# Kernel optimization log

Hardware: AMD Instinct MI355X
Metric: run time of the kernel (lower is better)

Reference implementation:

```python
import jax, jax.numpy as jnp
import numpy as np

K = 16  # kNN size (self included)
R = 4   # upsampling ratio


def _knn(pts, k):
    # pts: (B,N,3) -> idx (B,N,k); smallest distance first, so idx[:,:,0] is self
    sq = jnp.sum(pts * pts, axis=-1)
    d = sq[:, :, None] - 2.0 * jnp.einsum('bnd,bmd->bnm', pts, pts) + sq[:, None, :]
    _, idx = jax.lax.top_k(-d, k)
    return idx


def _gather(feats, idx):
    # feats (B,N,C), idx (B,N,k) -> (B,N,k,C)
    return jax.vmap(lambda f, i: f[i])(feats, idx)


def _conv1d(x, w, b):  # pointwise Conv1d: x (B,C,N)
    return jnp.einsum('oc,bcn->bon', w, x) + b[None, :, None]


def _conv2d(x, w, b):  # pointwise Conv2d: x (B,C,N,K)
    return jnp.einsum('oc,bcnk->bonk', w, x) + b[None, :, None, None]


def setup_inputs() -> dict:
    key = jax.random.key(0)
    ks = jax.random.split(key, 16)
    B, N = 2, 8192
    w = lambda k, s: jax.random.normal(k, s, jnp.float32) * 0.1
    return {
        'x': jax.random.normal(ks[0], (B, 3, N), jnp.float32),
        'mlp1_w1': w(ks[1], (32, 3)), 'mlp1_b1': jnp.zeros((32,), jnp.float32),
        'mlp1_w2': w(ks[2], (64, 32)), 'mlp1_b2': jnp.zeros((64,), jnp.float32),
        'mlp2_w1': w(ks[3], (32, 9)), 'mlp2_b1': jnp.zeros((32,), jnp.float32),
        'mlp3_w1': w(ks[4], (128, 96)), 'mlp3_b1': jnp.zeros((128,), jnp.float32),
        'mlp3_w2': w(ks[5], (12, 128)), 'mlp3_b2': jnp.zeros((12,), jnp.float32),
        'att_w1': w(ks[6], (128, 64)), 'att_b1': jnp.zeros((128,), jnp.float32),
        'att_w2': w(ks[7], (64, 128)), 'att_b2': jnp.zeros((64,), jnp.float32),
    }


def reference(x, mlp1_w1, mlp1_b1, mlp1_w2, mlp1_b2, mlp2_w1, mlp2_b1,
              mlp3_w1, mlp3_b1, mlp3_w2, mlp3_b2,
              att_w1, att_b1, att_w2, att_b2):
    B, C, N = x.shape
    pts = jnp.transpose(x, (0, 2, 1))                     # (B,N,3)
    idx = _knn(jax.lax.stop_gradient(pts), K)             # (B,N,K)

    # local 3x3 covariance features -> (B,9,N)
    nb = _gather(pts, idx)                                # (B,N,K,3)
    c = nb - jnp.mean(nb, axis=2, keepdims=True)
    cov = jnp.einsum('bnki,bnkj->bnij', c, c) / K         # (B,N,3,3)
    cov_feat = jnp.transpose(cov.reshape(B, N, 9), (0, 2, 1))

    # mlp1: 3 -> 32 -> 64, relu on both (last_act=True)
    f1 = jax.nn.relu(_conv1d(jax.nn.relu(_conv1d(x, mlp1_w1, mlp1_b1)), mlp1_w2, mlp1_b2))

    # gather neighbor features (exclude self) and form relative features
    fk = _gather(jnp.transpose(f1, (0, 2, 1)), idx[:, :, 1:])   # (B,N,K-1,64)
    f_knn = jnp.transpose(fk, (0, 3, 1, 2)) - f1[:, :, :, None]  # (B,64,N,K-1)

    # attention MLP (2D): 64 -> 128 -> 64, softmax over neighbor axis
    h = jax.nn.relu(_conv2d(f_knn, att_w1, att_b1))
    w = jax.nn.softmax(_conv2d(h, att_w2, att_b2), axis=-1)
    f_agg = jnp.sum(w * f_knn, axis=-1)                   # (B,64,N)

    # mlp2: 9 -> 32 with relu
    f_cov = jax.nn.relu(_conv1d(cov_feat, mlp2_w1, mlp2_b1))     # (B,32,N)

    f = jnp.concatenate([f_agg, f_cov], axis=1)           # (B,96,N)
    g = _conv1d(jax.nn.relu(_conv1d(f, mlp3_w1, mlp3_b1)), mlp3_w2, mlp3_b2)  # (B,3R,N)

    return jnp.tile(x, (1, 1, R)) + 0.15 * g.reshape(B, -1, R * N)
```

## Files before the change

### kernel.cpp

```cpp
#include <hip/hip_runtime.h>

#define BB 2
#define NN 8192
#define KK 16
#define QPB 64
#define PRE 256
#define CAP 10
typedef unsigned long long ull;
typedef unsigned short ushort;
#define KINF 0xFFFFFFFFFFFFFFFFULL

typedef __attribute__((ext_vector_type(8))) short short8;
typedef __attribute__((ext_vector_type(4))) float f32x4;

static __device__ __forceinline__ ushort f2bf(float f) {
    unsigned u = __float_as_uint(f);
    unsigned r = (u + 0x7FFFu + ((u >> 16) & 1u)) >> 16;
    return (ushort)r;
}
static __device__ __forceinline__ float bf2f(ushort s) {
    return __uint_as_float(((unsigned)s) << 16);
}

static __device__ __forceinline__ float distq(const float4& qp, const float4& cn) {
    return fmaf(qp.x, cn.x, fmaf(qp.y, cn.y, fmaf(qp.z, cn.z, __fadd_rn(qp.w, cn.w))));
}

__global__ __launch_bounds__(256) void prep_f1_kernel(
    const float* __restrict__ x, float4* __restrict__ pts4, float4* __restrict__ pts4n,
    const float* __restrict__ w1, const float* __restrict__ b1,
    const float* __restrict__ w2, const float* __restrict__ b2,
    ushort* __restrict__ f1)
{
    if (blockIdx.x < 64) {
        int t = blockIdx.x * 256 + threadIdx.x;
        int b = t >> 13, n = t & (NN - 1);
        float x0 = x[(b * 3 + 0) * NN + n];
        float x1 = x[(b * 3 + 1) * NN + n];
        float x2 = x[(b * 3 + 2) * NN + n];
        float sq = fmaf(x2, x2, fmaf(x1, x1, __fmul_rn(x0, x0)));
        pts4[t]  = make_float4(x0, x1, x2, sq);
        pts4n[t] = make_float4(-2.f * x0, -2.f * x1, -2.f * x2, sq);
    } else {
        int P = (blockIdx.x - 64) * 256 + threadIdx.x;
        int b = P >> 13, n = P & (NN - 1);
        float x0 = x[(b * 3 + 0) * NN + n];
        float x1 = x[(b * 3 + 1) * NN + n];
        float x2 = x[(b * 3 + 2) * NN + n];
        float h[32];
#pragma unroll
        for (int o = 0; o < 32; ++o) {
            float v = fmaf(w1[o * 3 + 2], x2, fmaf(w1[o * 3 + 1], x1, fmaf(w1[o * 3 + 0], x0, b1[o])));
            h[o] = fmaxf(v, 0.f);
        }
#pragma unroll
        for (int o4 = 0; o4 < 16; ++o4) {
            float vv[4];
#pragma unroll
            for (int u = 0; u < 4; ++u) {
                int o = o4 * 4 + u;
                float v = b2[o];
#pragma unroll
                for (int k = 0; k < 32; ++k) v = fmaf(w2[o * 32 + k], h[k], v);
                vv[u] = fmaxf(v, 0.f);
            }
            ushort4 s = { f2bf(vv[0]), f2bf(vv[1]), f2bf(vv[2]), f2bf(vv[3]) };
            *(ushort4*)(f1 + (size_t)P * 64 + o4 * 4) = s;
        }
    }
}

__global__ __launch_bounds__(512) void knn_prefix_kernel(
    const float4* __restrict__ pts4, const float4* __restrict__ pts4n,
    float* __restrict__ thrb)
{
    __shared__ float smem[8 * 4 * 64];

    const int t    = threadIdx.x;
    const int wv   = t >> 6;
    const int lane = t & 63;
    const int b    = blockIdx.y;
    const int q    = blockIdx.x * QPB + lane;
    const int sl   = __builtin_amdgcn_readfirstlane(wv);

    const float4 qp = pts4[b * NN + q];
    const float4* __restrict__ cp = pts4n + (size_t)b * NN + (size_t)sl * 1024;

    float l0 = 3.0e38f, l1 = 3.0e38f, l2 = 3.0e38f, l3 = 3.0e38f;

    for (int i0 = 0; i0 < PRE; i0 += 8) {
#pragma unroll
        for (int u = 0; u < 8; ++u) {
            float d = distq(qp, cp[i0 + u]);
            if (d < l3) {
                bool b2 = d < l2, b1 = d < l1, b0 = d < l0;
                l3 = b2 ? l2 : d;
                l2 = b2 ? (b1 ? l1 : d) : l2;
                l1 = b1 ? (b0 ? l0 : d) : l1;
                l0 = b0 ? d : l0;
            }
        }
    }

    smem[(wv * 4 + 0) * 64 + lane] = l0;
    smem[(wv * 4 + 1) * 64 + lane] = l1;
    smem[(wv * 4 + 2) * 64 + lane] = l2;
    smem[(wv * 4 + 3) * 64 + lane] = l3;
    __syncthreads();

    if (t < QPB) {
        float h[8];
        int kc[8];
#pragma unroll
        for (int s = 0; s < 8; ++s) { h[s] = smem[(s * 4) * 64 + t]; kc[s] = 0; }
        float best = 3.0e38f;
        for (int o = 0; o < KK; ++o) {
            best = h[0]; int bs = 0;
#pragma unroll
            for (int s = 1; s < 8; ++s) { if (h[s] < best) { best = h[s]; bs = s; } }
#pragma unroll
            for (int s = 0; s < 8; ++s) {
                if (s == bs) {
                    kc[s]++;
                    h[s] = (kc[s] < 4) ? smem[(s * 4 + kc[s]) * 64 + t] : 3.0e38f;
                }
            }
        }
        thrb[(size_t)b * NN + blockIdx.x * QPB + t] = best;
    }
}

__global__ __launch_bounds__(512) void knn_scan_kernel(
    const float4* __restrict__ pts4, const float4* __restrict__ pts4n,
    const float* __restrict__ thrb,
    ushort* __restrict__ buf, ushort* __restrict__ cnt)
{
    const int t    = threadIdx.x;
    const int wv   = t >> 6;
    const int lane = t & 63;
    const int b    = blockIdx.y;
    const int q    = blockIdx.x * QPB + lane;
    const int s    = __builtin_amdgcn_readfirstlane(blockIdx.z * 8 + wv);

    const float4 qp = pts4[b * NN + q];
    const float thr = thrb[(size_t)b * NN + q];
    const float4* __restrict__ cp = pts4n + (size_t)b * NN + (size_t)s * 256;
    const unsigned cbase = s * 256;

    const int cell = (((int)(b * NN) + q) << 5) + s;
    ushort* __restrict__ bp = buf + (size_t)cell * CAP;
    int pend = 0;

    for (int i0 = 0; i0 < 256; i0 += 8) {
#pragma unroll
        for (int u = 0; u < 8; ++u) {
            const int ci = i0 + u;
            float d = distq(qp, cp[ci]);
            if (d <= thr) {
                if (pend < CAP) bp[pend] = (ushort)(cbase + ci);
                pend++;
            }
        }
    }
    cnt[cell] = (ushort)((pend < CAP) ? pend : CAP);
}

__global__ __launch_bounds__(256) void knn_select_kernel(
    const float4* __restrict__ pts4, const float4* __restrict__ pts4n,
    const ushort* __restrict__ buf, const ushort* __restrict__ cnt,
    int* __restrict__ iout)
{
    __shared__ ull sm3[4][8][8][KK];

    const int t = threadIdx.x;
    const int wv = t >> 6, lane = t & 63;
    const int qq = lane & 7, hh = lane >> 3;
    const int q  = (blockIdx.x * 4 + wv) * 8 + qq;
    const int b  = q >> 13;

    const float4 qp = pts4[q];
    ull list[KK];
#pragma unroll
    for (int i = 0; i < KK; ++i) list[i] = KINF;

#pragma unroll
    for (int ss = 0; ss < 4; ++ss) {
        const int s = hh * 4 + ss;
        const int cell = (q << 5) + s;
        const int n = cnt[cell];
        const ushort* bp = buf + (size_t)cell * CAP;
        for (int i = 0; i < n; ++i) {
            int id = bp[i];
            float d = distq(qp, pts4n[b * NN + id]);
            unsigned ud = __float_as_uint(d);
            ud ^= ((unsigned)((int)ud >> 31)) | 0x80000000u;
            ull k = ((ull)ud << 32) | (unsigned)id;
#pragma unroll
            for (int i2 = KK - 1; i2 > 0; --i2) {
                bool c1 = k < list[i2];
                bool c2 = k < list[i2 - 1];
                ull nd = c2 ? list[i2 - 1] : k;
                list[i2] = c1 ? nd : list[i2];
            }
            list[0] = (k < list[0]) ? k : list[0];
        }
    }

#pragma unroll
    for (int k = 0; k < KK; ++k) sm3[wv][hh][qq][k] = list[k];

    if (hh == 0) {
        ull h[8]; int kc[8];
#pragma unroll
        for (int s = 0; s < 8; ++s) { h[s] = sm3[wv][s][qq][0]; kc[s] = 0; }
        int* op = iout + (size_t)q * KK;
        for (int o = 0; o < KK; ++o) {
            ull best = h[0]; int bs = 0;
#pragma unroll
            for (int s = 1; s < 8; ++s) { if (h[s] < best) { best = h[s]; bs = s; } }
            op[o] = (int)(unsigned)(best & 0xFFFFFFFFULL);
#pragma unroll
            for (int s = 0; s < 8; ++s) {
                if (s == bs) {
                    kc[s]++;
                    h[s] = (kc[s] < KK) ? sm3[wv][s][qq][kc[s]] : KINF;
                }
            }
        }
    }
}

__global__ __launch_bounds__(256, 2) void attn_cov_kernel(
    const ushort* __restrict__ f1, const int* __restrict__ idx,
    const float* __restrict__ aw1, const float* __restrict__ ab1,
    const float* __restrict__ aw2, const float* __restrict__ ab2,
    ushort* __restrict__ fagg,
    const float4* __restrict__ pts4,
    const float* __restrict__ cw, const float* __restrict__ cb,
    ushort* __restrict__ fcov)
{
    __shared__ __align__(16) ushort w1l[128][72];
    __shared__ __align__(16) ushort w2l[64][136];
    __shared__ __align__(16) ushort fkb[4][16][72];
    __shared__ __align__(16) ushort hb[4][16][136];

    const int t = threadIdx.x;

    if (blockIdx.x >= 512) {
        int P = (blockIdx.x - 512) * 256 + t;
        int b = P >> 13;
        const int4* ip4 = (const int4*)(idx + (size_t)P * KK);
        int ids[KK];
#pragma unroll
        for (int g = 0; g < 4; ++g) {
            int4 v = ip4[g];
            ids[g * 4 + 0] = v.x; ids[g * 4 + 1] = v.y;
            ids[g * 4 + 2] = v.z; ids[g * 4 + 3] = v.w;
        }
        float px[KK], py[KK], pz[KK];
#pragma unroll
        for (int k = 0; k < KK; ++k) {
            float4 c = pts4[b * NN + ids[k]];
            px[k] = c.x; py[k] = c.y; pz[k] = c.z;
        }
        float mx = 0.f, my = 0.f, mz = 0.f;
#pragma unroll
        for (int k = 0; k < KK; ++k) { mx += px[k]; my += py[k]; mz += pz[k]; }
        mx *= (1.f / 16.f); my *= (1.f / 16.f); mz *= (1.f / 16.f);
        float c00 = 0, c01 = 0, c02 = 0, c11 = 0, c12 = 0, c22 = 0;
#pragma unroll
        for (int k = 0; k < KK; ++k) {
            float dx = px[k] - mx, dy = py[k] - my, dz = pz[k] - mz;
            c00 = fmaf(dx, dx, c00); c01 = fmaf(dx, dy, c01); c02 = fmaf(dx, dz, c02);
            c11 = fmaf(dy, dy, c11); c12 = fmaf(dy, dz, c12); c22 = fmaf(dz, dz, c22);
        }
        const float inv = 1.f / 16.f;
        float cf[9] = { c00 * inv, c01 * inv, c02 * inv,
                        c01 * inv, c11 * inv, c12 * inv,
                        c02 * inv, c12 * inv, c22 * inv };
        ushort* outp = fcov + (size_t)P * 32;
#pragma unroll
        for (int o = 0; o < 32; ++o) {
            float v = cb[o];
#pragma unroll
            for (int m = 0; m < 9; ++m) v = fmaf(cw[o * 9 + m], cf[m], v);
            outp[o] = f2bf(fmaxf(v, 0.f));
        }
        return;
    }

    const int wv = t >> 6, lane = t & 63;
    const int l15 = lane & 15, qd = lane >> 4;

    for (int i = t; i < 128 * 64; i += 256) {
        int r = i >> 6, c = i & 63;
        w1l[r][c] = f2bf(aw1[i]);
    }
    for (int i = t; i < 64 * 128; i += 256) {
        int r = i >> 7, c = i & 127;
        w2l[r][c] = f2bf(aw2[i]);
    }
    __syncthreads();

    const int W = blockIdx.x * 4 + wv;
    for (int g = 0; g < 8; ++g) {
        const int P = W * 8 + g;
        const int b = P >> 13;

        float fc = bf2f(f1[(size_t)P * 64 + lane]);
        ushort fn[15];
#pragma unroll
        for (int j = 0; j < 15; ++j) {
            int nb = idx[(size_t)P * KK + 1 + j];
            fn[j] = f1[((size_t)b * NN + nb) * 64 + lane];
        }
#pragma unroll
        for (int j = 0; j < 15; ++j) fkb[wv][j][lane] = f2bf(bf2f(fn[j]) - fc);
        fkb[wv][15][lane] = 0;

        short8 a0 = *(const short8*)&fkb[wv][l15][qd * 8];
        short8 a1 = *(const short8*)&fkb[wv][l15][32 + qd * 8];

#pragma unroll
        for (int tile = 0; tile < 8; ++tile) {
            float bv = ab1[tile * 16 + l15];
            f32x4 acc = { bv, bv, bv, bv };
            short8 b0 = *(const short8*)&w1l[tile * 16 + l15][qd * 8];
            short8 b1f = *(const short8*)&w1l[tile * 16 + l15][32 + qd * 8];
            acc = __builtin_amdgcn_mfma_f32_16x16x32_bf16(a0, b0, acc, 0, 0, 0);
            acc = __builtin_amdgcn_mfma_f32_16x16x32_bf16(a1, b1f, acc, 0, 0, 0);
#pragma unroll
            for (int reg = 0; reg < 4; ++reg)
                hb[wv][qd * 4 + reg][tile * 16 + l15] = f2bf(fmaxf(acc[reg], 0.f));
        }

        short8 a2[4];
#pragma unroll
        for (int ks = 0; ks < 4; ++ks)
            a2[ks] = *(const short8*)&hb[wv][l15][ks * 32 + qd * 8];

        f32x4 L[4];
#pragma unroll
        for (int tile = 0; tile < 4; ++tile) {
            float bv = ab2[tile * 16 + l15];
            f32x4 acc = { bv, bv, bv, bv };
#pragma unroll
            for (int ks = 0; ks < 4; ++ks) {
                short8 bf = *(const short8*)&w2l[tile * 16 + l15][ks * 32 + qd * 8];
                acc = __builtin_amdgcn_mfma_f32_16x16x32_bf16(a2[ks], bf, acc, 0, 0, 0);
            }
            L[tile] = acc;
        }

        float fa[4];
#pragma unroll
        for (int tile = 0; tile < 4; ++tile) {
            float m1 = -3.0e38f;
#pragma unroll
            for (int reg = 0; reg < 4; ++reg)
                if (qd * 4 + reg < 15) m1 = fmaxf(m1, L[tile][reg]);
            m1 = fmaxf(m1, __shfl_xor(m1, 16));
            m1 = fmaxf(m1, __shfl_xor(m1, 32));
            float e[4], ssum = 0.f;
#pragma unroll
            for (int reg = 0; reg < 4; ++reg) {
                bool valid = (qd * 4 + reg < 15);
                e[reg] = valid ? __expf(L[tile][reg] - m1) : 0.f;
                ssum += e[reg];
            }
            ssum += __shfl_xor(ssum, 16);
            ssum += __shfl_xor(ssum, 32);
            float part = 0.f;
#pragma unroll
            for (int reg = 0; reg < 4; ++reg) {
                float fkv = bf2f(fkb[wv][qd * 4 + reg][tile * 16 + l15]);
                part = fmaf(e[reg], fkv, part);
            }
            part += __shfl_xor(part, 16);
            part += __shfl_xor(part, 32);
            fa[tile] = part / ssum;
        }
        if (qd == 0) {
#pragma unroll
            for (int tile = 0; tile < 4; ++tile)
                fagg[(size_t)P * 64 + tile * 16 + l15] = f2bf(fa[tile]);
        }
    }
}

__global__ __launch_bounds__(256) void mlp3_kernel(
    const ushort* __restrict__ fagg, const ushort* __restrict__ fcov,
    const float* __restrict__ w1, const float* __restrict__ b1,
    const float* __restrict__ w2, const float* __restrict__ b2,
    const float* __restrict__ x, float* __restrict__ out)
{
    __shared__ __align__(16) ushort fb[4][16][104];
    __shared__ __align__(16) ushort hb[4][16][136];

    const int t = threadIdx.x;
    const int wv = t >> 6, lane = t & 63;
    const int l15 = lane & 15, qd = lane >> 4;

    short8 w1f[8][3];
#pragma unroll
    for (int tile = 0; tile < 8; ++tile)
#pragma unroll
        for (int ks = 0; ks < 3; ++ks) {
            const float* p = w1 + ((size_t)(tile * 16 + l15) * 96 + ks * 32 + qd * 8);
            float4 A = *(const float4*)p, B = *(const float4*)(p + 4);
            short8 f;
            f[0] = f2bf(A.x); f[1] = f2bf(A.y); f[2] = f2bf(A.z); f[3] = f2bf(A.w);
            f[4] = f2bf(B.x); f[5] = f2bf(B.y); f[6] = f2bf(B.z); f[7] = f2bf(B.w);
            w1f[tile][ks] = f;
        }
    short8 w2f[4];
#pragma unroll
    for (int ks = 0; ks < 4; ++ks) {
        short8 f = {};
        if (l15 < 12) {
            const float* p = w2 + ((size_t)l15 * 128 + ks * 32 + qd * 8);
            float4 A = *(const float4*)p, B = *(const float4*)(p + 4);
            f[0] = f2bf(A.x); f[1] = f2bf(A.y); f[2] = f2bf(A.z); f[3] = f2bf(A.w);
            f[4] = f2bf(B.x); f[5] = f2bf(B.y); f[6] = f2bf(B.z); f[7] = f2bf(B.w);
        }
        w2f[ks] = f;
    }

    const int T = blockIdx.x * 4 + wv;

    {
        const int pt = lane >> 2, c4 = lane & 3;
        const ushort* fap = fagg + ((size_t)(T * 16 + pt) * 64 + c4 * 16);
        *(short8*)&fb[wv][pt][c4 * 16]     = *(const short8*)(fap);
        *(short8*)&fb[wv][pt][c4 * 16 + 8] = *(const short8*)(fap + 8);
        const ushort* fcp = fcov + ((size_t)(T * 16 + pt) * 32 + c4 * 8);
        *(short8*)&fb[wv][pt][64 + c4 * 8] = *(const short8*)(fcp);
    }

    short8 a[3];
#pragma unroll
    for (int ks = 0; ks < 3; ++ks)
        a[ks] = *(const short8*)&fb[wv][l15][ks * 32 + qd * 8];

#pragma unroll
    for (int tile = 0; tile < 8; ++tile) {
        float bv = b1[tile * 16 + l15];
        f32x4 acc = { bv, bv, bv, bv };
#pragma unroll
        for (int ks = 0; ks < 3; ++ks)
            acc = __builtin_amdgcn_mfma_f32_16x16x32_bf16(a[ks], w1f[tile][ks], acc, 0, 0, 0);
#pragma unroll
        for (int reg = 0; reg < 4; ++reg)
            hb[wv][qd * 4 + reg][tile * 16 + l15] = f2bf(fmaxf(acc[reg], 0.f));
    }

    short8 a2[4];
#pragma unroll
    for (int ks = 0; ks < 4; ++ks)
        a2[ks] = *(const short8*)&hb[wv][l15][ks * 32 + qd * 8];

    float bv2 = (l15 < 12) ? b2[l15] : 0.f;
    f32x4 acc = { bv2, bv2, bv2, bv2 };
#pragma unroll
    for (int ks = 0; ks < 4; ++ks)
        acc = __builtin_amdgcn_mfma_f32_16x16x32_bf16(a2[ks], w2f[ks], acc, 0, 0, 0);

    if (l15 < 12) {
        const int c = l15 >> 2, rr = l15 & 3;
#pragma unroll
        for (int reg = 0; reg < 4; ++reg) {
            int P = T * 16 + qd * 4 + reg;
            int b = P >> 13, n = P & (NN - 1);
            float xv = x[((size_t)b * 3 + c) * NN + n];
            out[(((size_t)b * 3 + c) * 4 + rr) * NN + n] = xv + 0.15f * acc[reg];
        }
    }
}

extern "C" void kernel_launch(void* const* d_in, const int* in_sizes, int n_in,
                              void* d_out, int out_size, void* d_ws, size_t ws_size,
                              hipStream_t stream)
{
    (void)in_sizes; (void)n_in; (void)out_size; (void)ws_size;
    const float* x    = (const float*)d_in[0];
    const float* m1w1 = (const float*)d_in[1];
    const float* m1b1 = (const float*)d_in[2];
    const float* m1w2 = (const float*)d_in[3];
    const float* m1b2 = (const float*)d_in[4];
    const float* m2w1 = (const float*)d_in[5];
    const float* m2b1 = (const float*)d_in[6];
    const float* m3w1 = (const float*)d_in[7];
    const float* m3b1 = (const float*)d_in[8];
    const float* m3w2 = (const float*)d_in[9];
    const float* m3b2 = (const float*)d_in[10];
    const float* aw1  = (const float*)d_in[11];
    const float* ab1  = (const float*)d_in[12];
    const float* aw2  = (const float*)d_in[13];
    const float* ab2  = (const float*)d_in[14];
    float* out = (float*)d_out;

    char* ws = (char*)d_ws;
    float4* pts4  = (float4*)(ws + 0);
    float4* pts4n = (float4*)(ws + 262144);
    float*  thrb  = (float*)(ws + 524288);
    int*    idxb  = (int*)  (ws + 589824);
    ushort* cntb  = (ushort*)(ws + 1638400);
    ushort* bufb  = (ushort*)(ws + 2686976);
    ushort* f1b   = (ushort*)(ws + 13172736);
    ushort* fagg  = (ushort*)(ws + 15269888);
    ushort* fcov  = (ushort*)(ws + 17367040);

    prep_f1_kernel<<<128, 256, 0, stream>>>(x, pts4, pts4n, m1w1, m1b1, m1w2, m1b2, f1b);
    knn_prefix_kernel<<<dim3(NN / QPB, BB), 512, 0, stream>>>(pts4, pts4n, thrb);
    knn_scan_kernel<<<dim3(NN / QPB, BB, 4), 512, 0, stream>>>(pts4, pts4n, thrb, bufb, cntb);
    knn_select_kernel<<<512, 256, 0, stream>>>(pts4, pts4n, bufb, cntb, idxb);
    attn_cov_kernel<<<576, 256, 0, stream>>>(f1b, idxb, aw1, ab1, aw2, ab2, fagg,
                                             pts4, m2w1, m2b1, fcov);
    mlp3_kernel<<<256, 256, 0, stream>>>(fagg, fcov, m3w1, m3b1, m3w2, m3b2, x, out);
}
```

Baseline: 269.0 us.

## Buffer prefix kNN candidates in LDS and batch top-4 insertion to cut divergence

```diff
diff --git a/kernel.cpp b/kernel.cpp
--- a/kernel.cpp
+++ b/kernel.cpp
@@ -5,7 +5,7 @@
 #define KK 16
 #define QPB 64
 #define PRE 256
-#define CAP 10
+#define CAP 16
 typedef unsigned long long ull;
 typedef unsigned short ushort;
 #define KINF 0xFFFFFFFFFFFFFFFFULL
@@ -74,6 +74,7 @@
     const float4* __restrict__ pts4, const float4* __restrict__ pts4n,
     float* __restrict__ thrb)
 {
+    __shared__ float pbuf[11 * 512];
     __shared__ float smem[8 * 4 * 64];
 
     const int t    = threadIdx.x;
@@ -87,21 +88,43 @@
     const float4* __restrict__ cp = pts4n + (size_t)b * NN + (size_t)sl * 1024;
 
     float l0 = 3.0e38f, l1 = 3.0e38f, l2 = 3.0e38f, l3 = 3.0e38f;
+    float curmax = 3.0e38f;
+    int pend = 0;
 
     for (int i0 = 0; i0 < PRE; i0 += 8) {
 #pragma unroll
         for (int u = 0; u < 8; ++u) {
             float d = distq(qp, cp[i0 + u]);
-            if (d < l3) {
-                bool b2 = d < l2, b1 = d < l1, b0 = d < l0;
-                l3 = b2 ? l2 : d;
-                l2 = b2 ? (b1 ? l1 : d) : l2;
-                l1 = b1 ? (b0 ? l0 : d) : l1;
-                l0 = b0 ? d : l0;
-            }
-        }
-    }
-
+            pbuf[pend * 512 + t] = d;
+            pend += (d < curmax) ? 1 : 0;
+        }
+        if (__any(pend >= 4)) {
+            for (int j = 0; j < 11; ++j) {
+                if (!__any(j < pend)) break;
+                float v = pbuf[j * 512 + t];
+                float k = (j < pend) ? v : 3.0e38f;
+                bool b3 = k < l3, b2 = k < l2, b1 = k < l1, b0 = k < l0;
+                l3 = b3 ? (b2 ? l2 : k) : l3;
+                l2 = b2 ? (b1 ? l1 : k) : l2;
+                l1 = b1 ? (b0 ? l0 : k) : l1;
+                l0 = b0 ? k : l0;
+            }
+            pend = 0;
+            curmax = l3;
+        }
+    }
+    for (int j = 0; j < 11; ++j) {
+        if (!__any(j < pend)) break;
+        float v = pbuf[j * 512 + t];
+        float k = (j < pend) ? v : 3.0e38f;
+        bool b3 = k < l3, b2 = k < l2, b1 = k < l1, b0 = k < l0;
+        l3 = b3 ? (b2 ? l2 : k) : l3;
+        l2 = b2 ? (b1 ? l1 : k) : l2;
+        l1 = b1 ? (b0 ? l0 : k) : l1;
+        l0 = b0 ? k : l0;
+    }
+
+    __syncthreads();
     smem[(wv * 4 + 0) * 64 + lane] = l0;
     smem[(wv * 4 + 1) * 64 + lane] = l1;
     smem[(wv * 4 + 2) * 64 + lane] = l2;
@@ -157,7 +180,7 @@
             const int ci = i0 + u;
             float d = distq(qp, cp[ci]);
             if (d <= thr) {
-                if (pend < CAP) bp[pend] = (ushort)(cbase + ci);
+                bp[pend & (CAP - 1)] = (ushort)(cbase + ci);
                 pend++;
             }
         }
@@ -506,9 +529,9 @@
     int*    idxb  = (int*)  (ws + 589824);
     ushort* cntb  = (ushort*)(ws + 1638400);
     ushort* bufb  = (ushort*)(ws + 2686976);
-    ushort* f1b   = (ushort*)(ws + 13172736);
-    ushort* fagg  = (ushort*)(ws + 15269888);
-    ushort* fcov  = (ushort*)(ws + 17367040);
+    ushort* f1b   = (ushort*)(ws + 19464192);
+    ushort* fagg  = (ushort*)(ws + 21561344);
+    ushort* fcov  = (ushort*)(ws + 23658496);
 
     prep_f1_kernel<<<128, 256, 0, stream>>>(x, pts4, pts4n, m1w1, m1b1, m1w2, m1b2, f1b);
     knn_prefix_kernel<<<dim3(NN / QPB, BB), 512, 0, stream>>>(pts4, pts4n, thrb);
```

Result: faster. 262.8 us (-2.3%).
